# Kernel optimization log

Hardware: AMD Instinct MI355X
Metric: run time of the kernel (lower is better)

The kernel has to match this reference:

```python
import jax, jax.numpy as jnp
import numpy as np

NHEAD = 16


def setup_inputs() -> dict:
    key = jax.random.key(0)
    ks = jax.random.split(key, 8)
    S, B, D = 2048, 2, 1024
    std = 1.0 / np.sqrt(D)
    src = jax.random.normal(ks[0], (S, B, D), dtype=jnp.float32)
    edge_bias_2d = jax.random.normal(ks[1], (S, S), dtype=jnp.float32)
    wq = jax.random.normal(ks[2], (D, D), dtype=jnp.float32) * std
    wk = jax.random.normal(ks[3], (D, D), dtype=jnp.float32) * std
    wv = jax.random.normal(ks[4], (D, D), dtype=jnp.float32) * std
    wo = jax.random.normal(ks[5], (D, D), dtype=jnp.float32) * std
    bq = jnp.zeros((D,), jnp.float32)
    bk = jnp.zeros((D,), jnp.float32)
    bv = jnp.zeros((D,), jnp.float32)
    bo = jnp.zeros((D,), jnp.float32)
    return {"src": src, "edge_bias_2d": edge_bias_2d, "wq": wq, "bq": bq,
            "wk": wk, "bk": bk, "wv": wv, "bv": bv, "wo": wo, "bo": bo}


def reference(src, edge_bias_2d, wq, bq, wk, bk, wv, bv, wo, bo):
    S, B, D = src.shape
    h = NHEAD
    hd = D // h
    scale = hd ** (-0.5)

    def heads(t):  # [S,B,D] -> [B,h,S,hd]
        return t.reshape(S, B, h, hd).transpose(1, 2, 0, 3)

    q = heads(src @ wq + bq)
    k = heads(src @ wk + bk)
    v = heads(src @ wv + bv)

    # [B,h,S,S]
    logits = jnp.einsum('bhsd,bhtd->bhst', q, k) * scale
    logits = logits + edge_bias_2d[None, None, :, :]
    attn = jax.nn.softmax(logits, axis=-1)
    # signed aggregation: sign(edge_bias) with 0 -> +1
    sign_gate = jnp.where(edge_bias_2d < 0, -1.0, 1.0).astype(attn.dtype)
    attn = attn * sign_gate[None, None, :, :]

    out = jnp.einsum('bhst,bhtd->bhsd', attn, v)  # [B,h,S,hd]
    out = out.transpose(2, 0, 1, 3).reshape(S, B, D)
    out = out @ wo + bo
    return out
```

## Files before the change

kernel.cpp:

```cpp
#include <hip/hip_runtime.h>
#include <stdint.h>

typedef unsigned short u16;
typedef unsigned int u32;

typedef __bf16 bf8 __attribute__((ext_vector_type(8)));
typedef bf8 bf8a __attribute__((may_alias));
typedef float f32x4 __attribute__((ext_vector_type(4)));
typedef uint2 uint2a __attribute__((may_alias));
typedef ushort4 ushort4a __attribute__((may_alias));
typedef float4 float4a __attribute__((may_alias));

#define MFMA_BF16(a, b, c) __builtin_amdgcn_mfma_f32_16x16x32_bf16((a), (b), (c), 0, 0, 0)

__device__ __forceinline__ u16 f2b(float x) {
  u32 u = __float_as_uint(x);
  return (u16)((u + 0x7fffu + ((u >> 16) & 1u)) >> 16);
}
__device__ __forceinline__ void async16(const u16* g, void* l) {
  __builtin_amdgcn_global_load_lds((const __attribute__((address_space(1))) u32*)g,
                                   (__attribute__((address_space(3))) u32*)l, 16, 0, 0);
}

__global__ __launch_bounds__(256) void prep_inputs(
    const float* __restrict__ src, u16* __restrict__ dst,
    const float* __restrict__ w0, const float* __restrict__ w1,
    const float* __restrict__ w2, const float* __restrict__ w3,
    u16* __restrict__ t0, u16* __restrict__ t1, u16* __restrict__ t2, u16* __restrict__ t3) {
  const int bid = blockIdx.x, tid = threadIdx.x;
  if (bid < 4096) {
    const int i = bid * 256 + tid;
    float4 v = *(const float4a*)(src + i * 4);
    ushort4 o;
    o.x = f2b(v.x); o.y = f2b(v.y); o.z = f2b(v.z); o.w = f2b(v.w);
    *(ushort4a*)(dst + i * 4) = o;
    return;
  }
  const int b2 = bid - 4096;
  const int z = b2 >> 8, xy = b2 & 255;
  const int bx = xy & 15, by = xy >> 4;
  const float* W = z == 0 ? w0 : z == 1 ? w1 : z == 2 ? w2 : w3;
  u16* T = z == 0 ? t0 : z == 1 ? t1 : z == 2 ? t2 : t3;
  __shared__ __align__(8) u16 tile[64][68];
  const int ty = tid >> 4, tx = tid & 15;
  const int kb = by * 64, nb = bx * 64;
#pragma unroll
  for (int i = 0; i < 4; ++i) {
    int lk = ty + i * 16;
    float4 v = *(const float4a*)(W + (kb + lk) * 1024 + nb + tx * 4);
    ushort4 h;
    h.x = f2b(v.x); h.y = f2b(v.y); h.z = f2b(v.z); h.w = f2b(v.w);
    *(ushort4a*)&tile[lk][tx * 4] = h;
  }
  __syncthreads();
#pragma unroll
  for (int i = 0; i < 4; ++i) {
    int ln = ty + i * 16;
    ushort4 v;
    v.x = tile[tx * 4 + 0][ln];
    v.y = tile[tx * 4 + 1][ln];
    v.z = tile[tx * 4 + 2][ln];
    v.w = tile[tx * 4 + 3][ln];
    *(ushort4a*)(T + (nb + ln) * 1024 + kb + tx * 4) = v;
  }
}

__global__ __launch_bounds__(256) void prep_eb(const float* __restrict__ EB,
                                               u16* __restrict__ E2) {
  const int gid = blockIdx.x * 256 + threadIdx.x;
  const int s = gid >> 9;
  const int t = (gid & 511) * 4;
  const float4 v = *(const float4a*)(EB + s * 2048 + t);
  const float c2 = 1.44269504088896340736f;
  ushort4 o;
  o.x = f2b(__builtin_amdgcn_exp2f(v.x * c2)) | (u16)((__float_as_uint(v.x) >> 16) & 0x8000u);
  o.y = f2b(__builtin_amdgcn_exp2f(v.y * c2)) | (u16)((__float_as_uint(v.y) >> 16) & 0x8000u);
  o.z = f2b(__builtin_amdgcn_exp2f(v.z * c2)) | (u16)((__float_as_uint(v.z) >> 16) & 0x8000u);
  o.w = f2b(__builtin_amdgcn_exp2f(v.w * c2)) | (u16)((__float_as_uint(v.w) >> 16) & 0x8000u);
  const int ti = ((s >> 4) * 128 + (t >> 4)) * 256 + (s & 15) * 16 + (t & 15);
  *(ushort4a*)(E2 + ti) = o;
}

__global__ __launch_bounds__(256) void gemm_bt(
    const u16* __restrict__ A,
    const u16* __restrict__ B0, const u16* __restrict__ B1, const u16* __restrict__ B2,
    const float* __restrict__ c0, const float* __restrict__ c1, const float* __restrict__ c2,
    float sc0, float sc1, float sc2,
    u16* __restrict__ O0, u16* __restrict__ O1, u16* __restrict__ O2,
    float* __restrict__ Of, int plain) {
  __shared__ __align__(16) u16 sm[8320];
  u16* As = sm;
  u16* Bs = sm + 4096;
  const int tid = threadIdx.x, lane = tid & 63, w = tid >> 6;
  const int wm = w >> 1, wn = w & 1, quad = lane >> 4, l16 = lane & 15;
  const int z = blockIdx.z;
  const u16* Bt = z == 0 ? B0 : (z == 1 ? B1 : B2);
  const float* bi = z == 0 ? c0 : (z == 1 ? c1 : c2);
  const float sc = z == 0 ? sc0 : (z == 1 ? sc1 : sc2);
  u16* O = z == 0 ? O0 : (z == 1 ? O1 : O2);
  const int row0 = blockIdx.y * 128, col0 = blockIdx.x * 128;

  f32x4 acc[4][4];
#pragma unroll
  for (int i = 0; i < 4; ++i)
#pragma unroll
    for (int j = 0; j < 4; ++j) acc[i][j] = f32x4{0.f, 0.f, 0.f, 0.f};

  const int e0 = tid, e1 = tid + 256;
  const int r0 = e0 >> 2, cc0 = (e0 & 3) * 8;
  const int r1 = e1 >> 2, cc1 = (e1 & 3) * 8;
  const u32 lb0 = (u32)(w * 64) * 16;
  const u32 lb1 = (u32)(w * 64 + 256) * 16;

  for (int k0 = 0; k0 < 1024; k0 += 32) {
    __syncthreads();
    async16(A + (row0 + r0) * 1024 + k0 + cc0, (char*)As + lb0);
    async16(A + (row0 + r1) * 1024 + k0 + cc1, (char*)As + lb1);
    async16(Bt + (col0 + r0) * 1024 + k0 + cc0, (char*)Bs + lb0);
    async16(Bt + (col0 + r1) * 1024 + k0 + cc1, (char*)Bs + lb1);
    __syncthreads();
    bf8a af[4], bfr[4];
#pragma unroll
    for (int i = 0; i < 4; ++i) {
      af[i] = *(const bf8a*)(As + (wm * 64 + i * 16 + l16) * 32 + quad * 8);
      bfr[i] = *(const bf8a*)(Bs + (wn * 64 + i * 16 + l16) * 32 + quad * 8);
    }
#pragma unroll
    for (int mt = 0; mt < 4; ++mt)
#pragma unroll
      for (int nt = 0; nt < 4; ++nt) acc[mt][nt] = MFMA_BF16(af[mt], bfr[nt], acc[mt][nt]);
  }

  if (!plain && z == 2) {
#pragma unroll
    for (int half = 0; half < 2; ++half) {
      __syncthreads();
      if (wn == half) {
#pragma unroll
        for (int nt = 0; nt < 4; ++nt) {
          const int el = nt * 16 + l16;
          const float bcol = bi[col0 + half * 64 + el];
#pragma unroll
          for (int mt = 0; mt < 4; ++mt) {
#pragma unroll
            for (int r = 0; r < 4; ++r) {
              const int lr = wm * 64 + mt * 16 + quad * 4 + r;
              sm[lr * 65 + el] = f2b((acc[mt][nt][r] + bcol) * sc);
            }
          }
        }
      }
      __syncthreads();
      const int hh = (col0 >> 6) + half;
#pragma unroll
      for (int j = 0; j < 4; ++j) {
        const int idx = j * 256 + tid;
        const int sg = idx & 7, el = (idx >> 3) & 63, b_ = idx >> 9;
        ushort4 oa, ob;
        {
          const int base = (2 * (sg * 8) + b_) * 65 + el;
          oa.x = sm[base + 0 * 130]; oa.y = sm[base + 1 * 130];
          oa.z = sm[base + 2 * 130]; oa.w = sm[base + 3 * 130];
          ob.x = sm[base + 4 * 130]; ob.y = sm[base + 5 * 130];
          ob.z = sm[base + 6 * 130]; ob.w = sm[base + 7 * 130];
        }
        u16* dst = O + ((size_t)((b_ * 16 + hh) * 64 + el)) * 2048 + (row0 >> 1) + sg * 8;
        *(ushort4a*)dst = oa;
        *(ushort4a*)(dst + 4) = ob;
      }
    }
    return;
  }

#pragma unroll
  for (int nt = 0; nt < 4; ++nt) {
    const int col = col0 + wn * 64 + nt * 16 + l16;
    const float bcol = bi[col];
#pragma unroll
    for (int mt = 0; mt < 4; ++mt) {
#pragma unroll
      for (int r = 0; r < 4; ++r) {
        const int rm = row0 + wm * 64 + mt * 16 + quad * 4 + r;
        const float fv = (acc[mt][nt][r] + bcol) * sc;
        if (plain) {
          Of[rm * 1024 + col] = fv;
        } else {
          const u16 hv = f2b(fv);
          const int s = rm >> 1, b_ = rm & 1, hh = col >> 6, e = col & 63;
          const int p = b_ * 16 + hh;
          O[(p * 2048 + s) * 64 + e] = hv;
        }
      }
    }
  }
}

#define STAGE_K(Ksbuf, kt_)                                                         \
  {                                                                                 \
    _Pragma("unroll") for (int c = 0; c < 4; ++c) {                                 \
      const int row_ = c * 32 + w * 8 + r8;                                         \
      async16(Kp + ((kt_) * 128 + row_) * 64 + c16s * 8,                            \
              (char*)(Ksbuf) + (c * 4 + w) * 1024);                                 \
    }                                                                               \
  }

#define ITER(KsC, KsN, vfP, vfC, kt_, FIRST, LAST)                                  \
  {                                                                                 \
    bf8a pf[4];                                                                     \
    if (!(FIRST)) {                                                                 \
      _Pragma("unroll") for (int st = 0; st < 4; ++st)                              \
        pf[st] = *(const bf8a*)(Pw + st * 1152 + l16 * 72 + quad * 16);             \
    }                                                                               \
    if (!(LAST)) STAGE_K(KsN, (kt_) + 1)                                            \
    uint2 ebt[4][2];            \
    {                                                                               \
      const int tb16_ = (kt_) * 8 + w * 2;                                          \
      _Pragma("unroll") for (int st = 0; st < 4; ++st)                              \
        _Pragma("unroll") for (int tt = 0; tt < 2; ++tt)                            \
          ebt[st][tt] = *(const uint2a*)(EBp + ((qt * 4 + st) * 128 + tb16_ + tt) * 256 \
                                         + l16 * 16 + quad * 4);                    \
    }                                                                               \
    bf8a kf[2][2];                                                                  \
    _Pragma("unroll") for (int tt = 0; tt < 2; ++tt) {                              \
      const int row_ = w * 32 + tt * 16 + l16;                 \
      _Pragma("unroll") for (int ks = 0; ks < 2; ++ks) {                            \
        const int cc_ = ((ks * 4 + quad) ^ (l16 & 7)) * 8;                          \
        kf[tt][ks] = *(const bf8a*)((KsC) + row_ * 64 + cc_);                       \
      }                                                                             \
    }                                                                               \
    f32x4 sacc[4][2];                                                               \
    __builtin_amdgcn_s_setprio(1);                                                  \
    _Pragma("unroll") for (int tt = 0; tt < 2; ++tt)                                \
      _Pragma("unroll") for (int st = 0; st < 4; ++st) {                            \
        f32x4 t0_ = f32x4{0.f, 0.f, 0.f, 0.f};                                      \
        t0_ = MFMA_BF16(kf[tt][0], qf[st][0], t0_);                                 \
        sacc[st][tt] = MFMA_BF16(kf[tt][1], qf[st][1], t0_);                        \
      }                                                                             \
    if (!(FIRST)) {           \
      _Pragma("unroll") for (int st = 0; st < 4; ++st)                              \
        _Pragma("unroll") for (int nt = 0; nt < 4; ++nt)                            \
          oacc[st][nt] = MFMA_BF16(vfP[nt], pf[st], oacc[st][nt]);                  \
    }                                                                               \
    __builtin_amdgcn_s_setprio(0);                                                  \
    _Pragma("unroll") for (int st = 0; st < 4; ++st) {                              \
      _Pragma("unroll") for (int tt = 0; tt < 2; ++tt) {                            \
        const uint2 e_ = ebt[st][tt];                                               \
        const float g0 = __uint_as_float(e_.x << 16);                               \
        const float g1 = __uint_as_float(e_.x & 0xffff0000u);                       \
        const float g2 = __uint_as_float(e_.y << 16);                               \
        const float g3 = __uint_as_float(e_.y & 0xffff0000u);                       \
        const float p0 = __builtin_amdgcn_exp2f(sacc[st][tt][0]) * g0;              \
        const float p1 = __builtin_amdgcn_exp2f(sacc[st][tt][1]) * g1;              \
        const float p2 = __builtin_amdgcn_exp2f(sacc[st][tt][2]) * g2;              \
        const float p3 = __builtin_amdgcn_exp2f(sacc[st][tt][3]) * g3;              \
        lsum[st] += (__builtin_fabsf(p0) + __builtin_fabsf(p1)) +                   \
                    (__builtin_fabsf(p2) + __builtin_fabsf(p3));                    \
        const u16 h0 = __builtin_bit_cast(u16, (__bf16)p0);                         \
        const u16 h1 = __builtin_bit_cast(u16, (__bf16)p1);                         \
        const u16 h2 = __builtin_bit_cast(u16, (__bf16)p2);                         \
        const u16 h3 = __builtin_bit_cast(u16, (__bf16)p3);                         \
        uint2 v_;                                                                   \
        v_.x = (u32)h0 | ((u32)h1 << 16);                                           \
        v_.y = (u32)h2 | ((u32)h3 << 16);                                           \
        *(uint2a*)(Pw + st * 1152 + l16 * 72 + tt * 32 + quad * 8) = v_;            \
      }                                                                             \
    }                                                                               \
    {                   \
      const int tb_ = (kt_) * 128 + w * 32;                                         \
      _Pragma("unroll") for (int nt = 0; nt < 4; ++nt)                              \
        vfC[nt] = *(const bf8a*)(Vp + (nt * 16 + l16) * 2048 + tb_ + quad * 8);     \
    }                                                                               \
    __syncthreads();                                                                \
  }

__global__ __launch_bounds__(256, 2) void attn_fused(
    const u16* __restrict__ Qw, const u16* __restrict__ Kw, const u16* __restrict__ Vw,
    const u16* __restrict__ EBp, u16* __restrict__ Ao) {
  __shared__ __align__(16) char smem[51456];
  u16* const Ks0 = (u16*)smem;
  u16* const Ks1 = (u16*)(smem + 16384);
  const int tid = threadIdx.x, lane = tid & 63, w = tid >> 6;
  const int quad = lane >> 4, l16 = lane & 15;
  const int id = blockIdx.x;
  const int xcd = id & 7, idx = id >> 3;
  const int pair = xcd * 4 + (idx & 3);
  const int qt = idx >> 2;
  const int bb = pair >> 4, hh = pair & 15;
  const u16* Qp = Qw + pair * (2048 * 64);
  const u16* Kp = Kw + pair * (2048 * 64);
  const u16* Vp = Vw + pair * (64 * 2048);
  const int s0 = qt * 64;
  char* const Pw = smem + 32768 + w * 4608;

  bf8a qf[4][2];
#pragma unroll
  for (int st = 0; st < 4; ++st)
#pragma unroll
    for (int ks = 0; ks < 2; ++ks)
      qf[st][ks] = *(const bf8a*)(Qp + (s0 + st * 16 + l16) * 64 + ks * 32 + quad * 8);

  f32x4 oacc[4][4];
#pragma unroll
  for (int i = 0; i < 4; ++i)
#pragma unroll
    for (int j = 0; j < 4; ++j) oacc[i][j] = f32x4{0.f, 0.f, 0.f, 0.f};
  float lsum[4] = {0.f, 0.f, 0.f, 0.f};

  const int r8 = lane >> 3;
  const int c16s = (lane & 7) ^ r8;

  bf8a vfA[4], vfB[4];

  STAGE_K(Ks0, 0)
  __syncthreads();

  ITER(Ks0, Ks1, vfA , vfA, 0, 1, 0)
  for (int kt = 1; kt < 14; kt += 2) {
    ITER(Ks1, Ks0, vfA, vfB, kt, 0, 0)
    ITER(Ks0, Ks1, vfB, vfA, kt + 1, 0, 0)
  }
  ITER(Ks1, Ks0, vfA, vfB, 15, 0, 1)
  {
    bf8a pf[4];
#pragma unroll
    for (int st = 0; st < 4; ++st)
      pf[st] = *(const bf8a*)(Pw + st * 1152 + l16 * 72 + quad * 16);
    __builtin_amdgcn_s_setprio(1);
#pragma unroll
    for (int st = 0; st < 4; ++st)
#pragma unroll
      for (int nt = 0; nt < 4; ++nt)
        oacc[st][nt] = MFMA_BF16(vfB[nt], pf[st], oacc[st][nt]);
    __builtin_amdgcn_s_setprio(0);
  }

  float* const Obuf = (float*)smem;
  float* const Lbuf = (float*)(smem + 51200);
#pragma unroll
  for (int st = 0; st < 4; ++st) {
    float ls = lsum[st];
    ls += __shfl_xor(ls, 16);
    ls += __shfl_xor(ls, 32);
    if (lane < 16) Lbuf[w * 16 + l16] = ls;
#pragma unroll
    for (int nt = 0; nt < 4; ++nt)
      *(float4a*)&Obuf[w * 1056 + l16 * 66 + nt * 16 + quad * 4] = (float4){
          oacc[st][nt][0], oacc[st][nt][1], oacc[st][nt][2], oacc[st][nt][3]};
    __syncthreads();
    {
      const int s_ = tid & 15, eg = (tid >> 4) * 4;
      float a0 = 0.f, a1 = 0.f, a2 = 0.f, a3 = 0.f;
#pragma unroll
      for (int wp = 0; wp < 4; ++wp) {
        const float4 x = *(const float4a*)&Obuf[wp * 1056 + s_ * 66 + eg];
        a0 += x.x; a1 += x.y; a2 += x.z; a3 += x.w;
      }
      const float lt = Lbuf[s_] + Lbuf[16 + s_] + Lbuf[32 + s_] + Lbuf[48 + s_];
      const float inv = 1.0f / lt;
      ushort4 o;
      o.x = f2b(a0 * inv); o.y = f2b(a1 * inv); o.z = f2b(a2 * inv); o.w = f2b(a3 * inv);
      *(ushort4a*)(Ao + ((s0 + st * 16 + s_) * 2 + bb) * 1024 + hh * 64 + eg) = o;
    }
    if (st < 3) __syncthreads();
  }
}

extern "C" void kernel_launch(void* const* d_in, const int* in_sizes, int n_in,
                              void* d_out, int out_size, void* d_ws, size_t ws_size,
                              hipStream_t stream) {
  const float* src = (const float*)d_in[0];
  const float* eb = (const float*)d_in[1];
  const float* wq = (const float*)d_in[2];
  const float* bq = (const float*)d_in[3];
  const float* wk = (const float*)d_in[4];
  const float* bk = (const float*)d_in[5];
  const float* wv = (const float*)d_in[6];
  const float* bv = (const float*)d_in[7];
  const float* wo = (const float*)d_in[8];
  const float* bo = (const float*)d_in[9];
  u16* ws = (u16*)d_ws;
  const size_t MM = 1024 * 1024;
  u16* wqT = ws;
  u16* wkT = ws + MM;
  u16* wvT = ws + 2 * MM;
  u16* woT = ws + 3 * MM;
  u16* srcB = ws + 4 * MM;
  u16* eb2 = ws + 4 * MM;
  u16* qW = ws + 8 * MM;
  u16* kW = ws + 12 * MM;
  u16* vW = ws + 16 * MM;
  u16* aO = ws + 20 * MM;
  float* out = (float*)d_out;
  const float c1 = 0.125f * 1.44269504088896340736f;

  prep_inputs<<<dim3(5120), 256, 0, stream>>>(src, srcB, wq, wk, wv, wo,
                                              wqT, wkT, wvT, woT);
  gemm_bt<<<dim3(8, 32, 3), 256, 0, stream>>>(srcB, wqT, wkT, wvT, bq, bk, bv,
                                              c1, 1.0f, 1.0f,
                                              qW, kW, vW, nullptr, 0);
  prep_eb<<<dim3(4096), 256, 0, stream>>>(eb, eb2);
  attn_fused<<<dim3(1024), 256, 0, stream>>>(qW, kW, vW, eb2, aO);
  gemm_bt<<<dim3(8, 32, 1), 256, 0, stream>>>(aO, woT, woT, woT, bo, bo, bo,
                                              1.0f, 1.0f, 1.0f,
                                              nullptr, nullptr, nullptr, out, 1);
}
```

Baseline: 276.2 us.

## Give each wave private K staging to drop per-iteration block barriers

The attention kernel now gives each wave its own double-buffered K slice in LDS, covering only the 32 key rows that wave consumes. This replaces the per-iteration __syncthreads with an explicit s_waitcnt vmcnt, and address arithmetic moves to incremented pointers. The V-projection GEMM also drops its LDS-transposed coalesced epilogue in favour of direct strided scalar stores. The aim is to remove block-wide synchronisation stalls in the attention loop, at the cost of uncoalesced 2-byte stores in the GEMM and a hand-tuned wait count that must match the number of outstanding loads.

New measurement: 251.1 us. 9.1% less time.

```diff
diff --git a/kernel.cpp b/kernel.cpp
--- a/kernel.cpp
+++ b/kernel.cpp
@@ -88,7 +88,7 @@
     float sc0, float sc1, float sc2,
     u16* __restrict__ O0, u16* __restrict__ O1, u16* __restrict__ O2,
     float* __restrict__ Of, int plain) {
-  __shared__ __align__(16) u16 sm[8320];
+  __shared__ __align__(16) u16 sm[8192];
   u16* As = sm;
   u16* Bs = sm + 4096;
   const int tid = threadIdx.x, lane = tid & 63, w = tid >> 6;
@@ -131,47 +131,6 @@
       for (int nt = 0; nt < 4; ++nt) acc[mt][nt] = MFMA_BF16(af[mt], bfr[nt], acc[mt][nt]);
   }
 
-  if (!plain && z == 2) {
-#pragma unroll
-    for (int half = 0; half < 2; ++half) {
-      __syncthreads();
-      if (wn == half) {
-#pragma unroll
-        for (int nt = 0; nt < 4; ++nt) {
-          const int el = nt * 16 + l16;
-          const float bcol = bi[col0 + half * 64 + el];
-#pragma unroll
-          for (int mt = 0; mt < 4; ++mt) {
-#pragma unroll
-            for (int r = 0; r < 4; ++r) {
-              const int lr = wm * 64 + mt * 16 + quad * 4 + r;
-              sm[lr * 65 + el] = f2b((acc[mt][nt][r] + bcol) * sc);
-            }
-          }
-        }
-      }
-      __syncthreads();
-      const int hh = (col0 >> 6) + half;
-#pragma unroll
-      for (int j = 0; j < 4; ++j) {
-        const int idx = j * 256 + tid;
-        const int sg = idx & 7, el = (idx >> 3) & 63, b_ = idx >> 9;
-        ushort4 oa, ob;
-        {
-          const int base = (2 * (sg * 8) + b_) * 65 + el;
-          oa.x = sm[base + 0 * 130]; oa.y = sm[base + 1 * 130];
-          oa.z = sm[base + 2 * 130]; oa.w = sm[base + 3 * 130];
-          ob.x = sm[base + 4 * 130]; ob.y = sm[base + 5 * 130];
-          ob.z = sm[base + 6 * 130]; ob.w = sm[base + 7 * 130];
-        }
-        u16* dst = O + ((size_t)((b_ * 16 + hh) * 64 + el)) * 2048 + (row0 >> 1) + sg * 8;
-        *(ushort4a*)dst = oa;
-        *(ushort4a*)(dst + 4) = ob;
-      }
-    }
-    return;
-  }
-
 #pragma unroll
   for (int nt = 0; nt < 4; ++nt) {
     const int col = col0 + wn * 64 + nt * 16 + l16;
@@ -188,46 +147,46 @@
           const u16 hv = f2b(fv);
           const int s = rm >> 1, b_ = rm & 1, hh = col >> 6, e = col & 63;
           const int p = b_ * 16 + hh;
-          O[(p * 2048 + s) * 64 + e] = hv;
+          if (z < 2) O[(p * 2048 + s) * 64 + e] = hv;
+          else O[(p * 64 + e) * 2048 + s] = hv;
         }
       }
     }
   }
 }
 
-#define STAGE_K(Ksbuf, kt_)                                                         \
+#define STAGE_K(Ksbuf)                                                              \
   {                                                                                 \
-    _Pragma("unroll") for (int c = 0; c < 4; ++c) {                                 \
-      const int row_ = c * 32 + w * 8 + r8;                                         \
-      async16(Kp + ((kt_) * 128 + row_) * 64 + c16s * 8,                            \
-              (char*)(Ksbuf) + (c * 4 + w) * 1024);                                 \
-    }                                                                               \
-  }
-
-#define ITER(KsC, KsN, vfP, vfC, kt_, FIRST, LAST)                                  \
+    _Pragma("unroll") for (int c = 0; c < 4; ++c)                                   \
+      async16(kpt + c * 512, (char*)(Ksbuf) + c * 1024);                            \
+    kpt += 8192;                                                                    \
+  }
+
+#define ITER(KsC, KsN, vfP, vfC, FIRST, LAST)                                       \
   {                                                                                 \
+             \
+                            \
+    asm volatile("s_waitcnt vmcnt(4)" ::: "memory");                                \
+    __builtin_amdgcn_sched_barrier(0);                                              \
     bf8a pf[4];                                                                     \
     if (!(FIRST)) {                                                                 \
       _Pragma("unroll") for (int st = 0; st < 4; ++st)                              \
         pf[st] = *(const bf8a*)(Pw + st * 1152 + l16 * 72 + quad * 16);             \
     }                                                                               \
-    if (!(LAST)) STAGE_K(KsN, (kt_) + 1)                                            \
-    uint2 ebt[4][2];            \
-    {                                                                               \
-      const int tb16_ = (kt_) * 8 + w * 2;                                          \
-      _Pragma("unroll") for (int st = 0; st < 4; ++st)                              \
-        _Pragma("unroll") for (int tt = 0; tt < 2; ++tt)                            \
-          ebt[st][tt] = *(const uint2a*)(EBp + ((qt * 4 + st) * 128 + tb16_ + tt) * 256 \
-                                         + l16 * 16 + quad * 4);                    \
-    }                                                                               \
     bf8a kf[2][2];                                                                  \
     _Pragma("unroll") for (int tt = 0; tt < 2; ++tt) {                              \
-      const int row_ = w * 32 + tt * 16 + l16;                 \
+      const int rl_ = tt * 16 + l16;                 \
       _Pragma("unroll") for (int ks = 0; ks < 2; ++ks) {                            \
         const int cc_ = ((ks * 4 + quad) ^ (l16 & 7)) * 8;                          \
-        kf[tt][ks] = *(const bf8a*)((KsC) + row_ * 64 + cc_);                       \
+        kf[tt][ks] = *(const bf8a*)((KsC) + rl_ * 64 + cc_);                        \
       }                                                                             \
     }                                                                               \
+    if (!(LAST)) STAGE_K(KsN)                                                       \
+    uint2 ebt[4][2];                                                                \
+    _Pragma("unroll") for (int st = 0; st < 4; ++st)                                \
+      _Pragma("unroll") for (int tt = 0; tt < 2; ++tt)                              \
+        ebt[st][tt] = *(const uint2a*)(ebpt + st * 32768 + tt * 256);               \
+    ebpt += 2048;                                                                   \
     f32x4 sacc[4][2];                                                               \
     __builtin_amdgcn_s_setprio(1);                                                  \
     _Pragma("unroll") for (int tt = 0; tt < 2; ++tt)                                \
@@ -265,20 +224,17 @@
         *(uint2a*)(Pw + st * 1152 + l16 * 72 + tt * 32 + quad * 8) = v_;            \
       }                                                                             \
     }                                                                               \
-    {                   \
-      const int tb_ = (kt_) * 128 + w * 32;                                         \
+    {            \
       _Pragma("unroll") for (int nt = 0; nt < 4; ++nt)                              \
-        vfC[nt] = *(const bf8a*)(Vp + (nt * 16 + l16) * 2048 + tb_ + quad * 8);     \
-    }                                                                               \
-    __syncthreads();                                                                \
+        vfC[nt] = *(const bf8a*)(vpt + nt * 32768);                                 \
+      vpt += 128;                                                                   \
+    }                                                                               \
   }
 
 __global__ __launch_bounds__(256, 2) void attn_fused(
     const u16* __restrict__ Qw, const u16* __restrict__ Kw, const u16* __restrict__ Vw,
     const u16* __restrict__ EBp, u16* __restrict__ Ao) {
   __shared__ __align__(16) char smem[51456];
-  u16* const Ks0 = (u16*)smem;
-  u16* const Ks1 = (u16*)(smem + 16384);
   const int tid = threadIdx.x, lane = tid & 63, w = tid >> 6;
   const int quad = lane >> 4, l16 = lane & 15;
   const int id = blockIdx.x;
@@ -290,6 +246,8 @@
   const u16* Kp = Kw + pair * (2048 * 64);
   const u16* Vp = Vw + pair * (64 * 2048);
   const int s0 = qt * 64;
+  u16* const Ks0 = (u16*)(smem + w * 8192);
+  u16* const Ks1 = (u16*)(smem + w * 8192 + 4096);
   char* const Pw = smem + 32768 + w * 4608;
 
   bf8a qf[4][2];
@@ -308,18 +266,22 @@
 
   const int r8 = lane >> 3;
   const int c16s = (lane & 7) ^ r8;
+  const u16* kpt = Kp + (w * 32 + r8) * 64 + c16s * 8;
+  const u16* ebpt = EBp + (qt * 4 * 128 + w * 2) * 256 + l16 * 16 + quad * 4;
+  const u16* vpt = Vp + l16 * 2048 + w * 32 + quad * 8;
 
   bf8a vfA[4], vfB[4];
 
-  STAGE_K(Ks0, 0)
-  __syncthreads();
-
-  ITER(Ks0, Ks1, vfA , vfA, 0, 1, 0)
-  for (int kt = 1; kt < 14; kt += 2) {
-    ITER(Ks1, Ks0, vfA, vfB, kt, 0, 0)
-    ITER(Ks0, Ks1, vfB, vfA, kt + 1, 0, 0)
-  }
-  ITER(Ks1, Ks0, vfA, vfB, 15, 0, 1)
+  STAGE_K(Ks0)
+  asm volatile("s_waitcnt vmcnt(0)" ::: "memory");
+  __builtin_amdgcn_sched_barrier(0);
+
+  ITER(Ks0, Ks1, vfA , vfA, 1, 0)
+  for (int it = 0; it < 7; ++it) {
+    ITER(Ks1, Ks0, vfA, vfB, 0, 0)
+    ITER(Ks0, Ks1, vfB, vfA, 0, 0)
+  }
+  ITER(Ks1, Ks0, vfA, vfB, 0, 1)
   {
     bf8a pf[4];
 #pragma unroll
@@ -334,6 +296,7 @@
     __builtin_amdgcn_s_setprio(0);
   }
 
+  __syncthreads();
   float* const Obuf = (float*)smem;
   float* const Lbuf = (float*)(smem + 51200);
 #pragma unroll
```
